# Performance work log

Hardware: AMD Instinct MI355X
Metric: run time of the kernel (lower is better)

The kernel has to match this reference:

```python
import jax, jax.numpy as jnp
import numpy as np

N = 50000
E = 800000
IN_C = 128
HID_C = 128
OUT_C = 128
N_CLS = 40


def setup_inputs() -> dict:
    key = jax.random.key(0)
    ks = jax.random.split(key, 12)
    x = jax.random.normal(ks[0], (N, IN_C), dtype=jnp.float32)
    edge_index = jax.random.randint(ks[1], (2, E), 0, N, dtype=jnp.int64)
    s = 1.0 / np.sqrt(IN_C)
    W_l1 = jax.random.uniform(ks[2], (IN_C, HID_C), jnp.float32, -s, s)
    W_r1 = jax.random.uniform(ks[3], (IN_C, HID_C), jnp.float32, -s, s)
    b1 = jax.random.uniform(ks[4], (HID_C,), jnp.float32, -s, s)
    s2 = 1.0 / np.sqrt(HID_C)
    W_l2 = jax.random.uniform(ks[5], (HID_C, OUT_C), jnp.float32, -s2, s2)
    W_r2 = jax.random.uniform(ks[6], (HID_C, OUT_C), jnp.float32, -s2, s2)
    b2 = jax.random.uniform(ks[7], (OUT_C,), jnp.float32, -s2, s2)
    s3 = 1.0 / np.sqrt(OUT_C)
    W_c = jax.random.uniform(ks[8], (OUT_C, N_CLS), jnp.float32, -s3, s3)
    b_c = jax.random.uniform(ks[9], (N_CLS,), jnp.float32, -s3, s3)
    return {"x": x, "edge_index": edge_index, "W_l1": W_l1, "W_r1": W_r1,
            "b1": b1, "W_l2": W_l2, "W_r2": W_r2, "b2": b2,
            "W_c": W_c, "b_c": b_c}


def _mean_aggregate(x, src, dst, deg_inv):
    # gather source node features over edges, scatter-mean to dst nodes
    msg = x[src]  # [E, C]
    agg = jax.ops.segment_sum(msg, dst, num_segments=N)  # [N, C]
    return agg * deg_inv[:, None]


def _sage_conv(x, src, dst, deg_inv, W_l, W_r, b):
    # PyG SAGEConv (mean aggr): out = agg @ W_l + x @ W_r + b
    agg = _mean_aggregate(x, src, dst, deg_inv)
    return agg @ W_l + x @ W_r + b


def reference(x, edge_index, W_l1, W_r1, b1, W_l2, W_r2, b2, W_c, b_c):
    src, dst = edge_index[0], edge_index[1]
    deg = jax.ops.segment_sum(jnp.ones((E,), jnp.float32), dst, num_segments=N)
    deg_inv = jnp.where(deg > 0, 1.0 / jnp.maximum(deg, 1.0), 0.0)
    h = jax.nn.relu(_sage_conv(x, src, dst, deg_inv, W_l1, W_r1, b1))
    h = jax.nn.relu(_sage_conv(h, src, dst, deg_inv, W_l2, W_r2, b2))
    return h @ W_c + b_c
```

## Files before the change

kernel.cpp:

```cpp
#include <hip/hip_runtime.h>

#define N_NODES 50000
#define N_EDGES 800000
#define C 128
#define NCLS 40
#define KB 98
#define BCAP 9216

typedef short bf16x8 __attribute__((ext_vector_type(8)));
typedef float f32x4 __attribute__((ext_vector_type(4)));
typedef unsigned short ushort_t;

__device__ __forceinline__ unsigned short f32_to_bf16(float f) {
    union { float f; unsigned u; } c; c.f = f;
    unsigned r = (c.u + 0x7FFFu + ((c.u >> 16) & 1u)) >> 16;
    return (unsigned short)r;
}
__device__ __forceinline__ float bf_lo(unsigned u) {
    union { unsigned u; float f; } c; c.u = u << 16; return c.f;
}
__device__ __forceinline__ float bf_hi(unsigned u) {
    union { unsigned u; float f; } c; c.u = u & 0xffff0000u; return c.f;
}
__device__ __forceinline__ unsigned pack_bf16(float lo, float hi) {
    return (unsigned)f32_to_bf16(lo) | ((unsigned)f32_to_bf16(hi) << 16);
}

__global__ __launch_bounds__(256)
void convert_all(const float* __restrict__ Wl1, const float* __restrict__ Wr1,
                 const float* __restrict__ Wl2, const float* __restrict__ Wr2,
                 const float* __restrict__ Wc,  const float* __restrict__ x,
                 ushort_t* __restrict__ Wbf1, ushort_t* __restrict__ Wbf2,
                 ushort_t* __restrict__ Wcb,  ushort_t* __restrict__ xb) {
    int b = blockIdx.x;
    int tid = threadIdx.x;
    if (b < 256) {
        const float* Wl = (b < 128) ? Wl1 : Wl2;
        const float* Wr = (b < 128) ? Wr1 : Wr2;
        ushort_t* Bpre  = (b < 128) ? Wbf1 : Wbf2;
        int idx = (b & 127) * 256 + tid;
        int n = idx >> 8;
        int k = idx & 255;
        float v = (k < 128) ? Wl[k * 128 + n] : Wr[(k - 128) * 128 + n];
        Bpre[n * 256 + k] = f32_to_bf16(v);
    } else if (b < 280) {
        int idx = (b - 256) * 256 + tid;
        if (idx < 48 * 128) {
            int n = idx >> 7;
            int k = idx & 127;
            float v = (n < NCLS) ? Wc[k * NCLS + n] : 0.f;
            Wcb[idx] = f32_to_bf16(v);
        }
    } else {
        int idx = (b - 280) * 256 + tid;
        const float4 v0 = *(const float4*)&x[idx * 8];
        const float4 v1 = *(const float4*)&x[idx * 8 + 4];
        uint4 o;
        o.x = pack_bf16(v0.x, v0.y);
        o.y = pack_bf16(v0.z, v0.w);
        o.z = pack_bf16(v1.x, v1.y);
        o.w = pack_bf16(v1.z, v1.w);
        ((uint4*)xb)[idx] = o;
    }
}

__global__ __launch_bounds__(256)
void bin_kernel(const int* __restrict__ src, const int* __restrict__ dst,
                int* __restrict__ bucket_cnt, unsigned* __restrict__ bucket_data) {
    __shared__ int lh[KB];
    int tid = threadIdx.x;
    int e0 = blockIdx.x * 4096;
    if (tid < KB) lh[tid] = 0;
    __syncthreads();
#pragma unroll
    for (int j = 0; j < 16; ++j) {
        int e = e0 + j * 256 + tid;
        if (e < N_EDGES) atomicAdd(&lh[dst[e] >> 9], 1);
    }
    __syncthreads();
    if (tid < KB) lh[tid] = atomicAdd(&bucket_cnt[tid], lh[tid]);
    __syncthreads();
#pragma unroll
    for (int j = 0; j < 16; ++j) {
        int e = e0 + j * 256 + tid;
        if (e < N_EDGES) {
            int d = dst[e];
            int b = d >> 9;
            int pos = atomicAdd(&lh[b], 1);
            if (pos < BCAP)
                bucket_data[b * BCAP + pos] = (unsigned)src[e] | ((unsigned)(d & 511) << 16);
        }
    }
}

__global__ __launch_bounds__(256)
void build_kernel(const int* __restrict__ bucket_cnt, const unsigned* __restrict__ bucket_data,
                  int* __restrict__ row_ptr, ushort_t* __restrict__ csr16) {
    __shared__ int wt[4];
    __shared__ int wt2[4];
    __shared__ int sbases[128];
    __shared__ int hist[512];
    __shared__ int loff[512];
    __shared__ ushort_t lcsr[BCAP];
    int tid = threadIdx.x;
    int b = blockIdx.x;
    int n0 = b << 9;
    int nb = min(512, N_NODES - n0);

    int v = 0, x = 0;
    if (tid < 128) {
        v = (tid < KB) ? bucket_cnt[tid] : 0;
        x = v;
#pragma unroll
        for (int off = 1; off < 64; off <<= 1) {
            int t = __shfl_up(x, off, 64);
            if ((tid & 63) >= off) x += t;
        }
        if ((tid & 63) == 63) wt[tid >> 6] = x;
    }
    hist[tid] = 0; hist[tid + 256] = 0;
    __syncthreads();
    if (tid < 128) sbases[tid] = x - v + ((tid >= 64) ? wt[0] : 0);
    __syncthreads();
    int base = sbases[b];
    int ecnt = min(bucket_cnt[b], BCAP);

    for (int i = tid; i < ecnt; i += 256)
        atomicAdd(&hist[bucket_data[b * BCAP + i] >> 16], 1);
    __syncthreads();

    int h0 = hist[2 * tid], h1 = hist[2 * tid + 1];
    int s = h0 + h1;
    int y = s;
#pragma unroll
    for (int off = 1; off < 64; off <<= 1) {
        int t = __shfl_up(y, off, 64);
        if ((tid & 63) >= off) y += t;
    }
    if ((tid & 63) == 63) wt2[tid >> 6] = y;
    __syncthreads();
    int add = 0;
    for (int j = 0; j < (tid >> 6); ++j) add += wt2[j];
    int ex = y + add - s;
    loff[2 * tid] = ex;
    loff[2 * tid + 1] = ex + h0;
    __syncthreads();

    for (int n = tid; n < nb; n += 256) row_ptr[n0 + n] = base + loff[n];
    if (b == KB - 1 && tid == 0) row_ptr[N_NODES] = N_EDGES;
    __syncthreads();

    for (int i = tid; i < ecnt; i += 256) {
        unsigned e = bucket_data[b * BCAP + i];
        int pos = atomicAdd(&loff[e >> 16], 1);
        lcsr[pos] = (ushort_t)(e & 0xFFFFu);
    }
    __syncthreads();
    for (int i = tid; i < ecnt; i += 256) csr16[base + i] = lcsr[i];
}

#define ALD 136
template<int CLS>
__global__ __launch_bounds__(256)
void fused_layer(const ushort_t* __restrict__ feat,
                 const int* __restrict__ row_ptr,
                 const ushort_t* __restrict__ csr16,
                 const ushort_t* __restrict__ Bpre,
                 const float* __restrict__ bias,
                 ushort_t* __restrict__ hout,
                 const ushort_t* __restrict__ Wcb,
                 const float* __restrict__ bc,
                 float* __restrict__ out) {
    __shared__ ushort_t aggL[64 * ALD];
    __shared__ ushort_t stg[64 * 40 + 128 * 40];
    ushort_t* AsX = stg;
    ushort_t* BsP = stg + 64 * 40;
    const int tid = threadIdx.x;
    const int r0 = blockIdx.x * 64;
    const int w = tid >> 6, lane = tid & 63, m = lane & 15, quad = lane >> 4;

    const uint4* fb = (const uint4*)feat;
    const int q = tid & 15;
    for (int p = 0; p < 4; ++p) {
        int nl = p * 16 + (tid >> 4);
        int node = r0 + nl;
        int beg = 0, end = 0;
        if (node < N_NODES) { beg = row_ptr[node]; end = row_ptr[node + 1]; }
        float a0[8], a1[8], a2[8], a3[8];
#pragma unroll
        for (int j = 0; j < 8; ++j) { a0[j] = 0.f; a1[j] = 0.f; a2[j] = 0.f; a3[j] = 0.f; }
        int i = beg;
        for (; i + 4 <= end; i += 4) {
            int s0 = csr16[i + 0];
            int s1 = csr16[i + 1];
            int s2 = csr16[i + 2];
            int s3 = csr16[i + 3];
            uint4 v0 = fb[s0 * 16 + q];
            uint4 v1 = fb[s1 * 16 + q];
            uint4 v2 = fb[s2 * 16 + q];
            uint4 v3 = fb[s3 * 16 + q];
            a0[0] += bf_lo(v0.x); a0[1] += bf_hi(v0.x); a0[2] += bf_lo(v0.y); a0[3] += bf_hi(v0.y);
            a0[4] += bf_lo(v0.z); a0[5] += bf_hi(v0.z); a0[6] += bf_lo(v0.w); a0[7] += bf_hi(v0.w);
            a1[0] += bf_lo(v1.x); a1[1] += bf_hi(v1.x); a1[2] += bf_lo(v1.y); a1[3] += bf_hi(v1.y);
            a1[4] += bf_lo(v1.z); a1[5] += bf_hi(v1.z); a1[6] += bf_lo(v1.w); a1[7] += bf_hi(v1.w);
            a2[0] += bf_lo(v2.x); a2[1] += bf_hi(v2.x); a2[2] += bf_lo(v2.y); a2[3] += bf_hi(v2.y);
            a2[4] += bf_lo(v2.z); a2[5] += bf_hi(v2.z); a2[6] += bf_lo(v2.w); a2[7] += bf_hi(v2.w);
            a3[0] += bf_lo(v3.x); a3[1] += bf_hi(v3.x); a3[2] += bf_lo(v3.y); a3[3] += bf_hi(v3.y);
            a3[4] += bf_lo(v3.z); a3[5] += bf_hi(v3.z); a3[6] += bf_lo(v3.w); a3[7] += bf_hi(v3.w);
        }
        int rem = end - i;
        if (rem > 0) {
            int s0 = csr16[i];
            int s1 = csr16[i + (rem > 1 ? 1 : 0)];
            int s2 = csr16[i + (rem > 2 ? 2 : 0)];
            uint4 v0 = fb[s0 * 16 + q];
            uint4 v1 = fb[s1 * 16 + q];
            uint4 v2 = fb[s2 * 16 + q];
            float m1 = rem > 1 ? 1.f : 0.f;
            float m2 = rem > 2 ? 1.f : 0.f;
            a0[0] += bf_lo(v0.x); a0[1] += bf_hi(v0.x); a0[2] += bf_lo(v0.y); a0[3] += bf_hi(v0.y);
            a0[4] += bf_lo(v0.z); a0[5] += bf_hi(v0.z); a0[6] += bf_lo(v0.w); a0[7] += bf_hi(v0.w);
            a1[0] += m1 * bf_lo(v1.x); a1[1] += m1 * bf_hi(v1.x); a1[2] += m1 * bf_lo(v1.y); a1[3] += m1 * bf_hi(v1.y);
            a1[4] += m1 * bf_lo(v1.z); a1[5] += m1 * bf_hi(v1.z); a1[6] += m1 * bf_lo(v1.w); a1[7] += m1 * bf_hi(v1.w);
            a2[0] += m2 * bf_lo(v2.x); a2[1] += m2 * bf_hi(v2.x); a2[2] += m2 * bf_lo(v2.y); a2[3] += m2 * bf_hi(v2.y);
            a2[4] += m2 * bf_lo(v2.z); a2[5] += m2 * bf_hi(v2.z); a2[6] += m2 * bf_lo(v2.w); a2[7] += m2 * bf_hi(v2.w);
        }
        int d = end - beg;
        float di = d > 0 ? 1.f / (float)d : 0.f;
        float r[8];
#pragma unroll
        for (int j = 0; j < 8; ++j) r[j] = (a0[j] + a1[j] + a2[j] + a3[j]) * di;
        uint4 o;
        o.x = pack_bf16(r[0], r[1]);
        o.y = pack_bf16(r[2], r[3]);
        o.z = pack_bf16(r[4], r[5]);
        o.w = pack_bf16(r[6], r[7]);
        *(uint4*)&aggL[nl * ALD + q * 8] = o;
    }
    __syncthreads();

    f32x4 acc[8];
#pragma unroll
    for (int t = 0; t < 8; ++t) acc[t] = (f32x4){0.f, 0.f, 0.f, 0.f};

    for (int kc = 0; kc < 8; ++kc) {
        if (kc) __syncthreads();
        if (kc >= 4) {
            int row = tid >> 2;
            int kq = tid & 3;
            int rg = r0 + row; if (rg >= N_NODES) rg = N_NODES - 1;
            uint4 v = *(const uint4*)&feat[rg * C + (kc & 3) * 32 + kq * 8];
            *(uint4*)&AsX[row * 40 + kq * 8] = v;
        }
#pragma unroll
        for (int i = 0; i < 2; ++i) {
            int slot = tid + i * 256;
            int n = slot >> 2;
            int qq = slot & 3;
            *(uint4*)&BsP[n * 40 + qq * 8] = *(const uint4*)&Bpre[n * 256 + kc * 32 + qq * 8];
        }
        __syncthreads();
        bf16x8 af = (kc < 4)
            ? *(const bf16x8*)&aggL[(w * 16 + m) * ALD + kc * 32 + quad * 8]
            : *(const bf16x8*)&AsX[(w * 16 + m) * 40 + quad * 8];
#pragma unroll
        for (int t = 0; t < 8; ++t) {
            bf16x8 bf = *(const bf16x8*)&BsP[(t * 16 + m) * 40 + quad * 8];
            acc[t] = __builtin_amdgcn_mfma_f32_16x16x32_bf16(af, bf, acc[t], 0, 0, 0);
        }
    }

    if (CLS == 0) {
#pragma unroll
        for (int t = 0; t < 8; ++t) {
            int colv = t * 16 + m;
            float bv = bias[colv];
#pragma unroll
            for (int reg = 0; reg < 4; ++reg) {
                int rg = r0 + w * 16 + quad * 4 + reg;
                if (rg < N_NODES) {
                    float vv = fmaxf(acc[t][reg] + bv, 0.f);
                    hout[rg * C + colv] = f32_to_bf16(vv);
                }
            }
        }
    } else {
        __syncthreads();
#pragma unroll
        for (int t = 0; t < 8; ++t) {
            int colv = t * 16 + m;
            float bv = bias[colv];
#pragma unroll
            for (int reg = 0; reg < 4; ++reg) {
                int rl = w * 16 + quad * 4 + reg;
                float vv = fmaxf(acc[t][reg] + bv, 0.f);
                aggL[rl * ALD + colv] = f32_to_bf16(vv);
            }
        }
#pragma unroll
        for (int i = 0; i < 3; ++i) {
            int slot = tid + i * 256;
            int n = slot >> 4, kq = slot & 15;
            uint4 vv = *(const uint4*)&Wcb[n * C + kq * 8];
            *(uint4*)&stg[(kq >> 2) * (48 * 40) + n * 40 + (kq & 3) * 8] = vv;
        }
        __syncthreads();
        f32x4 acc2[3];
#pragma unroll
        for (int t = 0; t < 3; ++t) acc2[t] = (f32x4){0.f, 0.f, 0.f, 0.f};
#pragma unroll
        for (int kc = 0; kc < 4; ++kc) {
            bf16x8 af = *(const bf16x8*)&aggL[(w * 16 + m) * ALD + kc * 32 + quad * 8];
#pragma unroll
            for (int t = 0; t < 3; ++t) {
                bf16x8 bf = *(const bf16x8*)&stg[kc * (48 * 40) + (t * 16 + m) * 40 + quad * 8];
                acc2[t] = __builtin_amdgcn_mfma_f32_16x16x32_bf16(af, bf, acc2[t], 0, 0, 0);
            }
        }
#pragma unroll
        for (int t = 0; t < 3; ++t) {
            int col = t * 16 + m;
            if (col < NCLS) {
                float bvv = bc[col];
#pragma unroll
                for (int reg = 0; reg < 4; ++reg) {
                    int rg = r0 + w * 16 + quad * 4 + reg;
                    if (rg < N_NODES) out[rg * NCLS + col] = acc2[t][reg] + bvv;
                }
            }
        }
    }
}

extern "C" void kernel_launch(void* const* d_in, const int* in_sizes, int n_in,
                              void* d_out, int out_size, void* d_ws, size_t ws_size,
                              hipStream_t stream) {
    const float* x   = (const float*)d_in[0];
    const int*   ei  = (const int*)d_in[1];
    const float* Wl1 = (const float*)d_in[2];
    const float* Wr1 = (const float*)d_in[3];
    const float* b1  = (const float*)d_in[4];
    const float* Wl2 = (const float*)d_in[5];
    const float* Wr2 = (const float*)d_in[6];
    const float* b2  = (const float*)d_in[7];
    const float* Wc  = (const float*)d_in[8];
    const float* bc  = (const float*)d_in[9];
    const int* srcI = ei;
    const int* dstI = ei + N_EDGES;
    float* out = (float*)d_out;

    ushort_t* xb   = (ushort_t*)d_ws;
    ushort_t* h1b  = xb + (size_t)N_NODES * C;
    ushort_t* Wbf1 = h1b + (size_t)N_NODES * C;
    ushort_t* Wbf2 = Wbf1 + 32768;
    ushort_t* Wcb  = Wbf2 + 32768;
    ushort_t* csr16 = Wcb + 6144;
    int* bucket_cnt = (int*)(csr16 + N_EDGES);
    int* row_ptr    = bucket_cnt + 128;
    unsigned* bucket_data = (unsigned*)(row_ptr + N_NODES + 1);

    convert_all<<<280 + (N_NODES * C / 8 + 255) / 256, 256, 0, stream>>>(
        Wl1, Wr1, Wl2, Wr2, Wc, x, Wbf1, Wbf2, Wcb, xb);

    hipMemsetAsync(bucket_cnt, 0, 128 * sizeof(int), stream);
    bin_kernel<<<(N_EDGES + 4095) / 4096, 256, 0, stream>>>(srcI, dstI, bucket_cnt, bucket_data);
    build_kernel<<<KB, 256, 0, stream>>>(bucket_cnt, bucket_data, row_ptr, csr16);

    fused_layer<0><<<(N_NODES + 63) / 64, 256, 0, stream>>>(
        xb, row_ptr, csr16, Wbf1, b1, h1b, nullptr, nullptr, nullptr);

    fused_layer<1><<<(N_NODES + 63) / 64, 256, 0, stream>>>(
        h1b, row_ptr, csr16, Wbf2, b2, nullptr, Wcb, bc, out);
}
```

Before: 207.7 us.

## Sort nodes by degree within buckets and prestage edge indices in LDS

The build kernel now counting-sorts the nodes of each 512-node bucket by in-degree into a permutation array. The fused layer kernels process nodes in that order, so the 16-lane groups of a wavefront see similar degrees and diverge less during gather. Each block also first copies up to 64 neighbor indices per node into shared memory, so the gather loop reads them with vector LDS loads instead of scalar global loads. In exchange it adds an extra sync and an indirect row lookup, scatters the output stores to permuted rows, and launches a few more blocks that hold padding entries.

```diff
diff --git a/kernel.cpp b/kernel.cpp
--- a/kernel.cpp
+++ b/kernel.cpp
@@ -95,12 +95,14 @@
 
 __global__ __launch_bounds__(256)
 void build_kernel(const int* __restrict__ bucket_cnt, const unsigned* __restrict__ bucket_data,
-                  int* __restrict__ row_ptr, ushort_t* __restrict__ csr16) {
+                  int* __restrict__ row_ptr, ushort_t* __restrict__ csr16,
+                  int* __restrict__ perm) {
     __shared__ int wt[4];
     __shared__ int wt2[4];
     __shared__ int sbases[128];
     __shared__ int hist[512];
     __shared__ int loff[512];
+    __shared__ int dhist[64];
     __shared__ ushort_t lcsr[BCAP];
     int tid = threadIdx.x;
     int b = blockIdx.x;
@@ -157,6 +159,28 @@
     }
     __syncthreads();
     for (int i = tid; i < ecnt; i += 256) csr16[base + i] = lcsr[i];
+
+    if (tid < 64) dhist[tid] = 0;
+    for (int p = tid; p < 512; p += 256) perm[(b << 9) + p] = -1;
+    __syncthreads();
+    int na = 2 * tid, nbb = 2 * tid + 1;
+    int c0 = min(h0, 63), c1 = min(h1, 63);
+    if (na < nb)  atomicAdd(&dhist[c0], 1);
+    if (nbb < nb) atomicAdd(&dhist[c1], 1);
+    __syncthreads();
+    if (tid < 64) {
+        int v2 = dhist[tid];
+        int xs = v2;
+#pragma unroll
+        for (int off = 1; off < 64; off <<= 1) {
+            int t = __shfl_up(xs, off, 64);
+            if (tid >= off) xs += t;
+        }
+        dhist[tid] = xs - v2;
+    }
+    __syncthreads();
+    if (na < nb)  { int pos = atomicAdd(&dhist[c0], 1); perm[(b << 9) + pos] = n0 + na; }
+    if (nbb < nb) { int pos = atomicAdd(&dhist[c1], 1); perm[(b << 9) + pos] = n0 + nbb; }
 }
 
 #define ALD 136
@@ -165,6 +189,7 @@
 void fused_layer(const ushort_t* __restrict__ feat,
                  const int* __restrict__ row_ptr,
                  const ushort_t* __restrict__ csr16,
+                 const int* __restrict__ perm,
                  const ushort_t* __restrict__ Bpre,
                  const float* __restrict__ bias,
                  ushort_t* __restrict__ hout,
@@ -173,32 +198,47 @@
                  float* __restrict__ out) {
     __shared__ ushort_t aggL[64 * ALD];
     __shared__ ushort_t stg[64 * 40 + 128 * 40];
+    __shared__ int tperm[64];
     ushort_t* AsX = stg;
     ushort_t* BsP = stg + 64 * 40;
+    ushort_t* eidx = stg;
     const int tid = threadIdx.x;
     const int r0 = blockIdx.x * 64;
     const int w = tid >> 6, lane = tid & 63, m = lane & 15, quad = lane >> 4;
+    const int q = tid & 15;
+    const int g = tid >> 4;
+
+    if (tid < 64) tperm[tid] = perm[r0 + tid];
+    __syncthreads();
+
+    for (int p = 0; p < 4; ++p) {
+        int nl = p * 16 + g;
+        int node = tperm[nl];
+        int beg = 0, end = 0;
+        if (node >= 0) { beg = row_ptr[node]; end = row_ptr[node + 1]; }
+        int dl = end - beg; if (dl > 64) dl = 64;
+        for (int j = q; j < dl; j += 16) eidx[nl * 64 + j] = csr16[beg + j];
+    }
+    __syncthreads();
 
     const uint4* fb = (const uint4*)feat;
-    const int q = tid & 15;
     for (int p = 0; p < 4; ++p) {
-        int nl = p * 16 + (tid >> 4);
-        int node = r0 + nl;
+        int nl = p * 16 + g;
+        int node = tperm[nl];
         int beg = 0, end = 0;
-        if (node < N_NODES) { beg = row_ptr[node]; end = row_ptr[node + 1]; }
+        if (node >= 0) { beg = row_ptr[node]; end = row_ptr[node + 1]; }
+        int deg = end - beg;
+        int dl = deg > 64 ? 64 : deg;
         float a0[8], a1[8], a2[8], a3[8];
 #pragma unroll
         for (int j = 0; j < 8; ++j) { a0[j] = 0.f; a1[j] = 0.f; a2[j] = 0.f; a3[j] = 0.f; }
-        int i = beg;
-        for (; i + 4 <= end; i += 4) {
-            int s0 = csr16[i + 0];
-            int s1 = csr16[i + 1];
-            int s2 = csr16[i + 2];
-            int s3 = csr16[i + 3];
-            uint4 v0 = fb[s0 * 16 + q];
-            uint4 v1 = fb[s1 * 16 + q];
-            uint4 v2 = fb[s2 * 16 + q];
-            uint4 v3 = fb[s3 * 16 + q];
+        int i = 0;
+        for (; i + 4 <= dl; i += 4) {
+            ushort4 s4 = *(const ushort4*)&eidx[nl * 64 + i];
+            uint4 v0 = fb[(int)s4.x * 16 + q];
+            uint4 v1 = fb[(int)s4.y * 16 + q];
+            uint4 v2 = fb[(int)s4.z * 16 + q];
+            uint4 v3 = fb[(int)s4.w * 16 + q];
             a0[0] += bf_lo(v0.x); a0[1] += bf_hi(v0.x); a0[2] += bf_lo(v0.y); a0[3] += bf_hi(v0.y);
             a0[4] += bf_lo(v0.z); a0[5] += bf_hi(v0.z); a0[6] += bf_lo(v0.w); a0[7] += bf_hi(v0.w);
             a1[0] += bf_lo(v1.x); a1[1] += bf_hi(v1.x); a1[2] += bf_lo(v1.y); a1[3] += bf_hi(v1.y);
@@ -208,11 +248,11 @@
             a3[0] += bf_lo(v3.x); a3[1] += bf_hi(v3.x); a3[2] += bf_lo(v3.y); a3[3] += bf_hi(v3.y);
             a3[4] += bf_lo(v3.z); a3[5] += bf_hi(v3.z); a3[6] += bf_lo(v3.w); a3[7] += bf_hi(v3.w);
         }
-        int rem = end - i;
+        int rem = dl - i;
         if (rem > 0) {
-            int s0 = csr16[i];
-            int s1 = csr16[i + (rem > 1 ? 1 : 0)];
-            int s2 = csr16[i + (rem > 2 ? 2 : 0)];
+            int s0 = eidx[nl * 64 + i];
+            int s1 = eidx[nl * 64 + i + (rem > 1 ? 1 : 0)];
+            int s2 = eidx[nl * 64 + i + (rem > 2 ? 2 : 0)];
             uint4 v0 = fb[s0 * 16 + q];
             uint4 v1 = fb[s1 * 16 + q];
             uint4 v2 = fb[s2 * 16 + q];
@@ -225,8 +265,13 @@
             a2[0] += m2 * bf_lo(v2.x); a2[1] += m2 * bf_hi(v2.x); a2[2] += m2 * bf_lo(v2.y); a2[3] += m2 * bf_hi(v2.y);
             a2[4] += m2 * bf_lo(v2.z); a2[5] += m2 * bf_hi(v2.z); a2[6] += m2 * bf_lo(v2.w); a2[7] += m2 * bf_hi(v2.w);
         }
-        int d = end - beg;
-        float di = d > 0 ? 1.f / (float)d : 0.f;
+        for (int j2 = 64; j2 < deg; ++j2) {
+            int s0 = csr16[beg + j2];
+            uint4 v0 = fb[s0 * 16 + q];
+            a0[0] += bf_lo(v0.x); a0[1] += bf_hi(v0.x); a0[2] += bf_lo(v0.y); a0[3] += bf_hi(v0.y);
+            a0[4] += bf_lo(v0.z); a0[5] += bf_hi(v0.z); a0[6] += bf_lo(v0.w); a0[7] += bf_hi(v0.w);
+        }
+        float di = deg > 0 ? 1.f / (float)deg : 0.f;
         float r[8];
 #pragma unroll
         for (int j = 0; j < 8; ++j) r[j] = (a0[j] + a1[j] + a2[j] + a3[j]) * di;
@@ -248,8 +293,8 @@
         if (kc >= 4) {
             int row = tid >> 2;
             int kq = tid & 3;
-            int rg = r0 + row; if (rg >= N_NODES) rg = N_NODES - 1;
-            uint4 v = *(const uint4*)&feat[rg * C + (kc & 3) * 32 + kq * 8];
+            int nd = tperm[row]; if (nd < 0) nd = 0;
+            uint4 v = *(const uint4*)&feat[nd * C + (kc & 3) * 32 + kq * 8];
             *(uint4*)&AsX[row * 40 + kq * 8] = v;
         }
 #pragma unroll
@@ -270,6 +315,10 @@
         }
     }
 
+    int prow[4];
+#pragma unroll
+    for (int reg = 0; reg < 4; ++reg) prow[reg] = tperm[w * 16 + quad * 4 + reg];
+
     if (CLS == 0) {
 #pragma unroll
         for (int t = 0; t < 8; ++t) {
@@ -277,8 +326,8 @@
             float bv = bias[colv];
 #pragma unroll
             for (int reg = 0; reg < 4; ++reg) {
-                int rg = r0 + w * 16 + quad * 4 + reg;
-                if (rg < N_NODES) {
+                int rg = prow[reg];
+                if (rg >= 0) {
                     float vv = fmaxf(acc[t][reg] + bv, 0.f);
                     hout[rg * C + colv] = f32_to_bf16(vv);
                 }
@@ -324,8 +373,8 @@
                 float bvv = bc[col];
 #pragma unroll
                 for (int reg = 0; reg < 4; ++reg) {
-                    int rg = r0 + w * 16 + quad * 4 + reg;
-                    if (rg < N_NODES) out[rg * NCLS + col] = acc2[t][reg] + bvv;
+                    int rg = prow[reg];
+                    if (rg >= 0) out[rg * NCLS + col] = acc2[t][reg] + bvv;
                 }
             }
         }
@@ -358,17 +407,18 @@
     int* bucket_cnt = (int*)(csr16 + N_EDGES);
     int* row_ptr    = bucket_cnt + 128;
     unsigned* bucket_data = (unsigned*)(row_ptr + N_NODES + 1);
+    int* perm = (int*)(bucket_data + (size_t)KB * BCAP);
 
     convert_all<<<280 + (N_NODES * C / 8 + 255) / 256, 256, 0, stream>>>(
         Wl1, Wr1, Wl2, Wr2, Wc, x, Wbf1, Wbf2, Wcb, xb);
 
     hipMemsetAsync(bucket_cnt, 0, 128 * sizeof(int), stream);
     bin_kernel<<<(N_EDGES + 4095) / 4096, 256, 0, stream>>>(srcI, dstI, bucket_cnt, bucket_data);
-    build_kernel<<<KB, 256, 0, stream>>>(bucket_cnt, bucket_data, row_ptr, csr16);
-
-    fused_layer<0><<<(N_NODES + 63) / 64, 256, 0, stream>>>(
-        xb, row_ptr, csr16, Wbf1, b1, h1b, nullptr, nullptr, nullptr);
-
-    fused_layer<1><<<(N_NODES + 63) / 64, 256, 0, stream>>>(
-        h1b, row_ptr, csr16, Wbf2, b2, nullptr, Wcb, bc, out);
-}
+    build_kernel<<<KB, 256, 0, stream>>>(bucket_cnt, bucket_data, row_ptr, csr16, perm);
+
+    fused_layer<0><<<KB * 8, 256, 0, stream>>>(
+        xb, row_ptr, csr16, perm, Wbf1, b1, h1b, nullptr, nullptr, nullptr);
+
+    fused_layer<1><<<KB * 8, 256, 0, stream>>>(
+        h1b, row_ptr, csr16, perm, Wbf2, b2, nullptr, Wcb, bc, out);
+}
```

Result: slower. 216.8 us (+4.4%).

## Gather neighbor features from FP8 copies to halve aggregation traffic

Applied to the files above, without the earlier changes.

Adds FP8 (e4m3) copies of the input features and the layer-1 output, and switches the neighbor mean-aggregation gather to read 8-byte FP8 vectors instead of 16-byte bf16 vectors. The bf16 copies are kept for the self term of the GEMM. The gather loop is also unrolled to 8 edges, with the next group's indices prefetched. This targets the random-gather memory traffic, which dominates. It adds extra writes of the quantized arrays and loses precision in the aggregated features.

```diff
diff --git a/kernel.cpp b/kernel.cpp
--- a/kernel.cpp
+++ b/kernel.cpp
@@ -9,21 +9,98 @@
 
 typedef short bf16x8 __attribute__((ext_vector_type(8)));
 typedef float f32x4 __attribute__((ext_vector_type(4)));
+typedef float f32x2 __attribute__((ext_vector_type(2)));
 typedef unsigned short ushort_t;
+typedef unsigned char uchar_t;
 
 __device__ __forceinline__ unsigned short f32_to_bf16(float f) {
     union { float f; unsigned u; } c; c.f = f;
     unsigned r = (c.u + 0x7FFFu + ((c.u >> 16) & 1u)) >> 16;
     return (unsigned short)r;
 }
-__device__ __forceinline__ float bf_lo(unsigned u) {
-    union { unsigned u; float f; } c; c.u = u << 16; return c.f;
-}
-__device__ __forceinline__ float bf_hi(unsigned u) {
-    union { unsigned u; float f; } c; c.u = u & 0xffff0000u; return c.f;
-}
 __device__ __forceinline__ unsigned pack_bf16(float lo, float hi) {
     return (unsigned)f32_to_bf16(lo) | ((unsigned)f32_to_bf16(hi) << 16);
+}
+
+#if defined(__has_builtin)
+#if __has_builtin(__builtin_amdgcn_cvt_pk_f32_fp8) && __has_builtin(__builtin_amdgcn_cvt_pk_fp8_f32)
+#define HAVE_FP8_CVT 1
+#endif
+#endif
+
+__device__ __forceinline__ float dec1m(unsigned b) {
+    unsigned s = (b & 0x80u) << 24;
+    unsigned em = b & 0x7fu;
+    if (em >= 8u) {
+        union { unsigned u; float f; } c; c.u = s | ((em + 960u) << 20); return c.f;
+    }
+    float r = (float)em * 0.001953125f;
+    return s ? -r : r;
+}
+__device__ __forceinline__ unsigned enc1m(float f) {
+    float a = fabsf(f);
+    unsigned s = f < 0.f ? 0x80u : 0u;
+    if (a >= 448.f) return s | 0x7Eu;
+    if (a < 0.0009765625f) return s;
+    int e; float m = frexpf(a, &e);
+    int E = e + 6;
+    unsigned q;
+    if (E >= 1) {
+        q = (unsigned)rintf(m * 16.f);
+        if (q >= 16u) { q = 8u; E += 1; }
+        if (E > 15) return s | 0x7Eu;
+        q = ((unsigned)E << 3) | (q - 8u);
+    } else {
+        q = (unsigned)rintf(a * 512.f);
+    }
+    return s | q;
+}
+
+__device__ __forceinline__ f32x2 dec_lo(unsigned w) {
+#ifdef HAVE_FP8_CVT
+    return __builtin_amdgcn_cvt_pk_f32_fp8((int)w, false);
+#else
+    f32x2 r; r[0] = dec1m(w & 0xffu); r[1] = dec1m((w >> 8) & 0xffu); return r;
+#endif
+}
+__device__ __forceinline__ f32x2 dec_hi(unsigned w) {
+#ifdef HAVE_FP8_CVT
+    return __builtin_amdgcn_cvt_pk_f32_fp8((int)w, true);
+#else
+    f32x2 r; r[0] = dec1m((w >> 16) & 0xffu); r[1] = dec1m((w >> 24) & 0xffu); return r;
+#endif
+}
+__device__ __forceinline__ unsigned enc4(float a, float b, float c, float d) {
+#ifdef HAVE_FP8_CVT
+    int r = 0;
+    r = __builtin_amdgcn_cvt_pk_fp8_f32(a, b, r, false);
+    r = __builtin_amdgcn_cvt_pk_fp8_f32(c, d, r, true);
+    return (unsigned)r;
+#else
+    return enc1m(a) | (enc1m(b) << 8) | (enc1m(c) << 16) | (enc1m(d) << 24);
+#endif
+}
+__device__ __forceinline__ uchar_t enc1(float f) {
+#ifdef HAVE_FP8_CVT
+    return (uchar_t)(__builtin_amdgcn_cvt_pk_fp8_f32(f, f, 0, false) & 0xff);
+#else
+    return (uchar_t)enc1m(f);
+#endif
+}
+
+__device__ __forceinline__ void accq(float* a, uint2 v) {
+    f32x2 p;
+    p = dec_lo(v.x); a[0] += p[0]; a[1] += p[1];
+    p = dec_hi(v.x); a[2] += p[0]; a[3] += p[1];
+    p = dec_lo(v.y); a[4] += p[0]; a[5] += p[1];
+    p = dec_hi(v.y); a[6] += p[0]; a[7] += p[1];
+}
+__device__ __forceinline__ void accqm(float* a, uint2 v, float mk) {
+    f32x2 p;
+    p = dec_lo(v.x); a[0] += mk * p[0]; a[1] += mk * p[1];
+    p = dec_hi(v.x); a[2] += mk * p[0]; a[3] += mk * p[1];
+    p = dec_lo(v.y); a[4] += mk * p[0]; a[5] += mk * p[1];
+    p = dec_hi(v.y); a[6] += mk * p[0]; a[7] += mk * p[1];
 }
 
 __global__ __launch_bounds__(256)
@@ -31,7 +108,8 @@
                  const float* __restrict__ Wl2, const float* __restrict__ Wr2,
                  const float* __restrict__ Wc,  const float* __restrict__ x,
                  ushort_t* __restrict__ Wbf1, ushort_t* __restrict__ Wbf2,
-                 ushort_t* __restrict__ Wcb,  ushort_t* __restrict__ xb) {
+                 ushort_t* __restrict__ Wcb,  ushort_t* __restrict__ xb,
+                 uchar_t* __restrict__ xq) {
     int b = blockIdx.x;
     int tid = threadIdx.x;
     if (b < 256) {
@@ -61,6 +139,10 @@
         o.z = pack_bf16(v1.x, v1.y);
         o.w = pack_bf16(v1.z, v1.w);
         ((uint4*)xb)[idx] = o;
+        uint2 q8;
+        q8.x = enc4(v0.x, v0.y, v0.z, v0.w);
+        q8.y = enc4(v1.x, v1.y, v1.z, v1.w);
+        ((uint2*)xq)[idx] = q8;
     }
 }
 
@@ -162,12 +244,14 @@
 #define ALD 136
 template<int CLS>
 __global__ __launch_bounds__(256)
-void fused_layer(const ushort_t* __restrict__ feat,
+void fused_layer(const uchar_t* __restrict__ featq,
+                 const ushort_t* __restrict__ feat,
                  const int* __restrict__ row_ptr,
                  const ushort_t* __restrict__ csr16,
                  const ushort_t* __restrict__ Bpre,
                  const float* __restrict__ bias,
                  ushort_t* __restrict__ hout,
+                 uchar_t* __restrict__ houtq,
                  const ushort_t* __restrict__ Wcb,
                  const float* __restrict__ bc,
                  float* __restrict__ out) {
@@ -179,54 +263,64 @@
     const int r0 = blockIdx.x * 64;
     const int w = tid >> 6, lane = tid & 63, m = lane & 15, quad = lane >> 4;
 
-    const uint4* fb = (const uint4*)feat;
+    const uint2* fq = (const uint2*)featq;
     const int q = tid & 15;
     for (int p = 0; p < 4; ++p) {
         int nl = p * 16 + (tid >> 4);
         int node = r0 + nl;
         int beg = 0, end = 0;
         if (node < N_NODES) { beg = row_ptr[node]; end = row_ptr[node + 1]; }
+        int deg = end - beg;
         float a0[8], a1[8], a2[8], a3[8];
 #pragma unroll
         for (int j = 0; j < 8; ++j) { a0[j] = 0.f; a1[j] = 0.f; a2[j] = 0.f; a3[j] = 0.f; }
-        int i = beg;
-        for (; i + 4 <= end; i += 4) {
-            int s0 = csr16[i + 0];
-            int s1 = csr16[i + 1];
-            int s2 = csr16[i + 2];
-            int s3 = csr16[i + 3];
-            uint4 v0 = fb[s0 * 16 + q];
-            uint4 v1 = fb[s1 * 16 + q];
-            uint4 v2 = fb[s2 * 16 + q];
-            uint4 v3 = fb[s3 * 16 + q];
-            a0[0] += bf_lo(v0.x); a0[1] += bf_hi(v0.x); a0[2] += bf_lo(v0.y); a0[3] += bf_hi(v0.y);
-            a0[4] += bf_lo(v0.z); a0[5] += bf_hi(v0.z); a0[6] += bf_lo(v0.w); a0[7] += bf_hi(v0.w);
-            a1[0] += bf_lo(v1.x); a1[1] += bf_hi(v1.x); a1[2] += bf_lo(v1.y); a1[3] += bf_hi(v1.y);
-            a1[4] += bf_lo(v1.z); a1[5] += bf_hi(v1.z); a1[6] += bf_lo(v1.w); a1[7] += bf_hi(v1.w);
-            a2[0] += bf_lo(v2.x); a2[1] += bf_hi(v2.x); a2[2] += bf_lo(v2.y); a2[3] += bf_hi(v2.y);
-            a2[4] += bf_lo(v2.z); a2[5] += bf_hi(v2.z); a2[6] += bf_lo(v2.w); a2[7] += bf_hi(v2.w);
-            a3[0] += bf_lo(v3.x); a3[1] += bf_hi(v3.x); a3[2] += bf_lo(v3.y); a3[3] += bf_hi(v3.y);
-            a3[4] += bf_lo(v3.z); a3[5] += bf_hi(v3.z); a3[6] += bf_lo(v3.w); a3[7] += bf_hi(v3.w);
+
+        int n8 = deg >> 3;
+        int s0 = 0, s1 = 0, s2 = 0, s3 = 0, s4 = 0, s5 = 0, s6 = 0, s7 = 0;
+        if (n8 > 0) {
+            s0 = csr16[beg];     s1 = csr16[beg + 1]; s2 = csr16[beg + 2]; s3 = csr16[beg + 3];
+            s4 = csr16[beg + 4]; s5 = csr16[beg + 5]; s6 = csr16[beg + 6]; s7 = csr16[beg + 7];
+        }
+        for (int it = 0; it < n8; ++it) {
+            uint2 v0 = fq[s0 * 16 + q];
+            uint2 v1 = fq[s1 * 16 + q];
+            uint2 v2 = fq[s2 * 16 + q];
+            uint2 v3 = fq[s3 * 16 + q];
+            uint2 v4 = fq[s4 * 16 + q];
+            uint2 v5 = fq[s5 * 16 + q];
+            uint2 v6 = fq[s6 * 16 + q];
+            uint2 v7 = fq[s7 * 16 + q];
+            if (it + 1 < n8) {
+                int bs = beg + (it + 1) * 8;
+                s0 = csr16[bs];     s1 = csr16[bs + 1]; s2 = csr16[bs + 2]; s3 = csr16[bs + 3];
+                s4 = csr16[bs + 4]; s5 = csr16[bs + 5]; s6 = csr16[bs + 6]; s7 = csr16[bs + 7];
+            }
+            accq(a0, v0); accq(a1, v1); accq(a2, v2); accq(a3, v3);
+            accq(a0, v4); accq(a1, v5); accq(a2, v6); accq(a3, v7);
+        }
+        int i = beg + n8 * 8;
+        if (i + 4 <= end) {
+            int t0 = csr16[i], t1 = csr16[i + 1], t2 = csr16[i + 2], t3 = csr16[i + 3];
+            uint2 v0 = fq[t0 * 16 + q];
+            uint2 v1 = fq[t1 * 16 + q];
+            uint2 v2 = fq[t2 * 16 + q];
+            uint2 v3 = fq[t3 * 16 + q];
+            accq(a0, v0); accq(a1, v1); accq(a2, v2); accq(a3, v3);
+            i += 4;
         }
         int rem = end - i;
         if (rem > 0) {
-            int s0 = csr16[i];
-            int s1 = csr16[i + (rem > 1 ? 1 : 0)];
-            int s2 = csr16[i + (rem > 2 ? 2 : 0)];
-            uint4 v0 = fb[s0 * 16 + q];
-            uint4 v1 = fb[s1 * 16 + q];
-            uint4 v2 = fb[s2 * 16 + q];
-            float m1 = rem > 1 ? 1.f : 0.f;
-            float m2 = rem > 2 ? 1.f : 0.f;
-            a0[0] += bf_lo(v0.x); a0[1] += bf_hi(v0.x); a0[2] += bf_lo(v0.y); a0[3] += bf_hi(v0.y);
-            a0[4] += bf_lo(v0.z); a0[5] += bf_hi(v0.z); a0[6] += bf_lo(v0.w); a0[7] += bf_hi(v0.w);
-            a1[0] += m1 * bf_lo(v1.x); a1[1] += m1 * bf_hi(v1.x); a1[2] += m1 * bf_lo(v1.y); a1[3] += m1 * bf_hi(v1.y);
-            a1[4] += m1 * bf_lo(v1.z); a1[5] += m1 * bf_hi(v1.z); a1[6] += m1 * bf_lo(v1.w); a1[7] += m1 * bf_hi(v1.w);
-            a2[0] += m2 * bf_lo(v2.x); a2[1] += m2 * bf_hi(v2.x); a2[2] += m2 * bf_lo(v2.y); a2[3] += m2 * bf_hi(v2.y);
-            a2[4] += m2 * bf_lo(v2.z); a2[5] += m2 * bf_hi(v2.z); a2[6] += m2 * bf_lo(v2.w); a2[7] += m2 * bf_hi(v2.w);
-        }
-        int d = end - beg;
-        float di = d > 0 ? 1.f / (float)d : 0.f;
+            int t0 = csr16[i];
+            int t1 = csr16[i + (rem > 1 ? 1 : 0)];
+            int t2 = csr16[i + (rem > 2 ? 2 : 0)];
+            uint2 v0 = fq[t0 * 16 + q];
+            uint2 v1 = fq[t1 * 16 + q];
+            uint2 v2 = fq[t2 * 16 + q];
+            accq(a0, v0);
+            accqm(a1, v1, rem > 1 ? 1.f : 0.f);
+            accqm(a2, v2, rem > 2 ? 1.f : 0.f);
+        }
+        float di = deg > 0 ? 1.f / (float)deg : 0.f;
         float r[8];
 #pragma unroll
         for (int j = 0; j < 8; ++j) r[j] = (a0[j] + a1[j] + a2[j] + a3[j]) * di;
@@ -281,6 +375,7 @@
                 if (rg < N_NODES) {
                     float vv = fmaxf(acc[t][reg] + bv, 0.f);
                     hout[rg * C + colv] = f32_to_bf16(vv);
+                    houtq[rg * C + colv] = enc1(vv);
                 }
             }
         }
@@ -358,17 +453,19 @@
     int* bucket_cnt = (int*)(csr16 + N_EDGES);
     int* row_ptr    = bucket_cnt + 128;
     unsigned* bucket_data = (unsigned*)(row_ptr + N_NODES + 1);
+    uchar_t* xq = (uchar_t*)(((uintptr_t)(bucket_data + (size_t)KB * BCAP) + 255) & ~(uintptr_t)255);
+    uchar_t* h1q = xq + (size_t)N_NODES * C;
 
     convert_all<<<280 + (N_NODES * C / 8 + 255) / 256, 256, 0, stream>>>(
-        Wl1, Wr1, Wl2, Wr2, Wc, x, Wbf1, Wbf2, Wcb, xb);
+        Wl1, Wr1, Wl2, Wr2, Wc, x, Wbf1, Wbf2, Wcb, xb, xq);
 
     hipMemsetAsync(bucket_cnt, 0, 128 * sizeof(int), stream);
     bin_kernel<<<(N_EDGES + 4095) / 4096, 256, 0, stream>>>(srcI, dstI, bucket_cnt, bucket_data);
     build_kernel<<<KB, 256, 0, stream>>>(bucket_cnt, bucket_data, row_ptr, csr16);
 
     fused_layer<0><<<(N_NODES + 63) / 64, 256, 0, stream>>>(
-        xb, row_ptr, csr16, Wbf1, b1, h1b, nullptr, nullptr, nullptr);
+        xq, xb, row_ptr, csr16, Wbf1, b1, h1b, h1q, nullptr, nullptr, nullptr);
 
     fused_layer<1><<<(N_NODES + 63) / 64, 256, 0, stream>>>(
-        h1b, row_ptr, csr16, Wbf2, b2, nullptr, Wcb, bc, out);
-}
+        h1q, h1b, row_ptr, csr16, Wbf2, b2, nullptr, nullptr, Wcb, bc, out);
+}
```

New measurement: 221.0 us. +6.4%, slower.
